# Kernel tuning notes

Measured on AMD Instinct MI355X. Metric: run time of the kernel, lower is better.

Reference implementation:

```python
import jax, jax.numpy as jnp
import numpy as np

N_PER_CLOUD = 2048   # points per cloud (batch entries are equal-sized, sorted)
NUM_CLOUDS = 8       # batch_size constant in the source module
RADIUS = 0.2         # init arg r
MAX_NEIGHBORS = 32   # init arg max_neighbors
F_IN, H1, H2, F_OUT = 3, 64, 64, 128  # PointNet++ SA MLP widths; nn input = F_IN + 3


def setup_inputs() -> dict:
    key = jax.random.key(0)
    ks = jax.random.split(key, 8)
    N = NUM_CLOUDS * N_PER_CLOUD
    x = jax.random.normal(ks[0], (N, F_IN), dtype=jnp.float32)
    pos = jax.random.uniform(ks[1], (N, 3), dtype=jnp.float32)  # unit cube
    batch = jnp.repeat(jnp.arange(NUM_CLOUDS, dtype=jnp.int32), N_PER_CLOUD)
    d_in = F_IN + 3
    W1 = jax.random.normal(ks[2], (d_in, H1), dtype=jnp.float32) / np.sqrt(d_in)
    b1 = jnp.zeros((H1,), dtype=jnp.float32)
    W2 = jax.random.normal(ks[3], (H1, H2), dtype=jnp.float32) / np.sqrt(H1)
    b2 = jnp.zeros((H2,), dtype=jnp.float32)
    W3 = jax.random.normal(ks[4], (H2, F_OUT), dtype=jnp.float32) / np.sqrt(H2)
    b3 = jnp.zeros((F_OUT,), dtype=jnp.float32)
    return dict(x=x, pos=pos, batch=batch, W1=W1, b1=b1, W2=W2, b2=b2, W3=W3, b3=b3)


def reference(x, pos, batch, W1, b1, W2, b2, W3, b3):
    N = pos.shape[0]
    B = N // N_PER_CLOUD
    n = N_PER_CLOUD
    posb = pos.reshape(B, n, 3)
    xb = x.reshape(B, n, -1)

    # --- radius ball query (per cloud, first MAX_NEIGHBORS in index order) ---
    diff = posb[:, :, None, :] - posb[:, None, :, :]          # [B, n_query, n_src, 3]
    d2 = jnp.sum(diff * diff, axis=-1)                        # [B, n, n]
    valid = d2 <= RADIUS * RADIUS                             # includes self -> >=1 nbr
    j_idx = jnp.arange(n, dtype=jnp.int32)
    keys = jnp.where(valid, j_idx[None, None, :], n)          # invalid -> sentinel n
    nbr = jnp.argsort(keys, axis=-1)[..., :MAX_NEIGHBORS]     # [B, n, K]
    nbr_ok = jnp.take_along_axis(keys, nbr, axis=-1) < n      # [B, n, K] bool

    # --- PointNetConv: msg = nn(cat([x_j, pos_j - pos_i])), max aggregation ---
    b_ix = jnp.arange(B)[:, None, None]
    x_j = xb[b_ix, nbr]                                        # [B, n, K, F_IN]
    rel = posb[b_ix, nbr] - posb[:, :, None, :]               # [B, n, K, 3]
    msg = jnp.concatenate([x_j, rel], axis=-1)                # [B, n, K, F_IN+3]
    h = jax.nn.relu(msg @ W1 + b1)
    h = jax.nn.relu(h @ W2 + b2)
    h = h @ W3 + b3                                           # [B, n, K, F_OUT]
    h = jnp.where(nbr_ok[..., None], h, -jnp.inf)
    out = jnp.max(h, axis=2).reshape(N, -1)                   # [N, F_OUT]
    return out, pos, batch
```

## Files before the change

### kernel.cpp

```cpp
#include <hip/hip_runtime.h>
#include <hip/hip_bf16.h>
#include <math.h>

#define NPC   2048
#define NC    8
#define NTOT  (NPC * NC)
#define KMAX  32
#define R2    0.04f

typedef short bf16x8  __attribute__((ext_vector_type(8)));
typedef float f32x16  __attribute__((ext_vector_type(16)));

__device__ __forceinline__ unsigned int f2bf(float f) {
    unsigned int u = __float_as_uint(f);
    return (u + 0x7FFFu + ((u >> 16) & 1u)) >> 16;
}

__device__ __forceinline__ unsigned int pkbf(float a, float b) {
    unsigned int r;
    asm("v_cvt_pk_bf16_f32 %0, %1, %2" : "=v"(r) : "v"(a), "v"(b));
    return r;
}

__device__ __forceinline__ int mbcnt64(unsigned long long m) {
    return (int)__builtin_amdgcn_mbcnt_hi((unsigned int)(m >> 32),
            __builtin_amdgcn_mbcnt_lo((unsigned int)m, 0u));
}

__device__ __forceinline__ bf16x8 mk_frag(const f32x16& a, int off) {
    int4 w;
    w.x = (int)pkbf(fmaxf(a[off+0],0.f), fmaxf(a[off+1],0.f));
    w.y = (int)pkbf(fmaxf(a[off+2],0.f), fmaxf(a[off+3],0.f));
    w.z = (int)pkbf(fmaxf(a[off+4],0.f), fmaxf(a[off+5],0.f));
    w.w = (int)pkbf(fmaxf(a[off+6],0.f), fmaxf(a[off+7],0.f));
    return __builtin_bit_cast(bf16x8, w);
}

__global__ __launch_bounds__(512) void prep_small(
    const float* __restrict__ pos, const int* __restrict__ batch,
    const float* __restrict__ W1, const float* __restrict__ b1,
    const float* __restrict__ W2, const float* __restrict__ b2,
    const float* __restrict__ W3,
    unsigned short* __restrict__ wf, float* __restrict__ out)
{
    int b = blockIdx.x, tid = threadIdx.x;
    if (b < 28) {
        int g = b * 512 + tid;
        if (g < 1024) {
            int j = g & 7, lane = (g >> 3) & 63, t = g >> 9;
            int k = (lane >> 5)*8 + j, ch = t*32 + (lane & 31);
            float v = (k < 6) ? W1[k*64 + ch] : (k == 6 ? b1[ch] : 0.f);
            wf[g] = (unsigned short)f2bf(v);
        } else if (g < 6144) {
            int g2 = g - 1024;
            int j = g2 & 7, lane = (g2 >> 3) & 63, f = g2 >> 9;
            int t = f / 5, kk = f % 5;
            int hi = lane >> 5, row = t*32 + (lane & 31);
            float v;
            if (kk < 4) {
                int k = (j & 3) + 4*hi + 8*(2*(kk & 1) + (j >> 2)) + 32*(kk >> 1);
                v = W2[k*64 + row];
            } else {
                v = (hi == 0 && j == 0) ? b2[row] : 0.f;
            }
            wf[g] = (unsigned short)f2bf(v);
        } else {
            int g3 = g - 6144;
            int j = g3 & 7, lane = (g3 >> 3) & 63, f = g3 >> 9;
            int n = f >> 2, kk = f & 3;
            int hi = lane >> 5, col = n*32 + (lane & 31);
            int k = (j & 3) + 4*hi + 8*(2*(kk & 1) + (j >> 2)) + 32*(kk >> 1);
            wf[g] = (unsigned short)f2bf(W3[k*128 + col]);
        }
    } else {
        int i = (b - 28) * 512 + tid;
        if (i < NTOT*3) out[NTOT*128 + i] = pos[i];
        else            out[NTOT*131 + (i - NTOT*3)] = (float)batch[i - NTOT*3];
    }
}

__global__ __launch_bounds__(1024, 8) void fused_kernel(
    const float* __restrict__ x, const float* __restrict__ pos,
    const unsigned short* __restrict__ wf, const float* __restrict__ b3,
    float* __restrict__ out)
{
    __shared__ float2 sPxy[NPC];
    __shared__ float  sPz[NPC];
    __shared__ int4   sW[1664];
    __shared__ int    snbr[16*32];

    const int tid  = threadIdx.x;
    const int lane = tid & 63, wave = tid >> 6;
    const int e = lane & 31, hi = lane >> 5;
    const int q     = blockIdx.x * 16 + wave;
    const int base  = (q >> 11) << 11;
    const int ql    = q - base;

    if (tid < 512) {
        const float4* src = (const float4*)(pos + 3*base);
        float4 f0 = src[3*tid], f1 = src[3*tid+1], f2 = src[3*tid+2];
        sPxy[4*tid+0] = make_float2(f0.x, f0.y); sPz[4*tid+0] = f0.z;
        sPxy[4*tid+1] = make_float2(f0.w, f1.x); sPz[4*tid+1] = f1.y;
        sPxy[4*tid+2] = make_float2(f1.z, f1.w); sPz[4*tid+2] = f2.x;
        sPxy[4*tid+3] = make_float2(f2.y, f2.z); sPz[4*tid+3] = f2.w;
    } else {
        const int4* wsrc = (const int4*)(wf + 1024);
        int t = tid - 512;
        #pragma unroll
        for (int it = 0; it < 4; ++it) {
            int idx = it*512 + t;
            if (idx < 1664) sW[idx] = wsrc[idx];
        }
    }
    bf16x8 wA1_0 = *(const bf16x8*)(wf + (0*64 + lane)*8);
    bf16x8 wA1_1 = *(const bf16x8*)(wf + (1*64 + lane)*8);
    float b3v[4];
    #pragma unroll
    for (int n = 0; n < 4; ++n) b3v[n] = b3[n*32 + e];
    __syncthreads();

    const float2 qxy = sPxy[ql];
    const float qx = qxy.x, qy = qxy.y, qz = sPz[ql];
    int cnt = 0;
    for (int j0 = 0; j0 < NPC && cnt < KMAX; j0 += 256) {
        unsigned long long ms[4];
        bool vs[4];
        #pragma unroll
        for (int s = 0; s < 4; ++s) {
            int j = j0 + s*64 + lane;
            float2 pxy = sPxy[j];
            float  pz  = sPz[j];
            float dx = __fsub_rn(pxy.x, qx);
            float dy = __fsub_rn(pxy.y, qy);
            float dz = __fsub_rn(pz,    qz);
            float d2 = __fadd_rn(__fadd_rn(__fmul_rn(dx,dx), __fmul_rn(dy,dy)),
                                 __fmul_rn(dz,dz));
            vs[s] = d2 <= R2;
            ms[s] = __ballot(vs[s]);
        }
        #pragma unroll
        for (int s = 0; s < 4; ++s) {
            int slot = cnt + mbcnt64(ms[s]);
            if (vs[s] && slot < KMAX) snbr[(wave << 5) + slot] = j0 + s*64 + lane;
            cnt += (int)__popcll(ms[s]);
        }
    }
    if (cnt > KMAX) cnt = KMAX;

    int jl = (e < cnt) ? snbr[(wave << 5) + e] : ql;
    float2 pjxy = sPxy[jl];
    float  pjz  = sPz[jl];
    float xj0 = x[3*(base + jl)], xj1 = x[3*(base + jl) + 1], xj2 = x[3*(base + jl) + 2];

    const unsigned int one_w = pkbf(1.0f, 0.0f);
    int4 ow = {0,0,0,0};
    if (!hi) ow.x = (int)one_w;
    const bf16x8 onef = __builtin_bit_cast(bf16x8, ow);

    float r0 = pjxy.x - qx, r1 = pjxy.y - qy, r2 = pjz - qz;
    int4 mw;
    mw.x = hi ? 0 : (int)pkbf(xj0, xj1);
    mw.y = hi ? 0 : (int)pkbf(xj2, r0);
    mw.z = hi ? 0 : (int)pkbf(r1, r2);
    mw.w = hi ? 0 : (int)one_w;
    bf16x8 msgf = __builtin_bit_cast(bf16x8, mw);

    __builtin_amdgcn_s_setprio(1);
    f32x16 acc0 = {}, acc1 = {};
    acc0 = __builtin_amdgcn_mfma_f32_32x32x16_bf16(wA1_0, msgf, acc0, 0, 0, 0);
    acc1 = __builtin_amdgcn_mfma_f32_32x32x16_bf16(wA1_1, msgf, acc1, 0, 0, 0);
    __builtin_amdgcn_s_setprio(0);
    bf16x8 h1f[4];
    h1f[0] = mk_frag(acc0, 0);
    h1f[1] = mk_frag(acc0, 8);
    h1f[2] = mk_frag(acc1, 0);
    h1f[3] = mk_frag(acc1, 8);

    __builtin_amdgcn_s_setprio(1);
    f32x16 c20 = {}, c21 = {};
    #pragma unroll
    for (int kk = 0; kk < 4; ++kk) {
        c20 = __builtin_amdgcn_mfma_f32_32x32x16_bf16(
                *(const bf16x8*)&sW[(0*5 + kk)*64 + lane], h1f[kk], c20, 0, 0, 0);
        c21 = __builtin_amdgcn_mfma_f32_32x32x16_bf16(
                *(const bf16x8*)&sW[(1*5 + kk)*64 + lane], h1f[kk], c21, 0, 0, 0);
    }
    c20 = __builtin_amdgcn_mfma_f32_32x32x16_bf16(
            *(const bf16x8*)&sW[(0*5 + 4)*64 + lane], onef, c20, 0, 0, 0);
    c21 = __builtin_amdgcn_mfma_f32_32x32x16_bf16(
            *(const bf16x8*)&sW[(1*5 + 4)*64 + lane], onef, c21, 0, 0, 0);
    __builtin_amdgcn_s_setprio(0);
    bf16x8 h2f[4];
    h2f[0] = mk_frag(c20, 0);
    h2f[1] = mk_frag(c20, 8);
    h2f[2] = mk_frag(c21, 0);
    h2f[3] = mk_frag(c21, 8);

    const bool full = (cnt == 32);
    #pragma unroll
    for (int n = 0; n < 4; ++n) {
        __builtin_amdgcn_s_setprio(1);
        f32x16 c = {};
        #pragma unroll
        for (int kk = 0; kk < 4; ++kk)
            c = __builtin_amdgcn_mfma_f32_32x32x16_bf16(
                    h2f[kk], *(const bf16x8*)&sW[640 + (n*4 + kk)*64 + lane], c, 0, 0, 0);
        __builtin_amdgcn_s_setprio(0);
        float m;
        if (full) {
            float t0 = fmaxf(fmaxf(c[0],  c[1]),  c[2]);
            float t1 = fmaxf(fmaxf(c[3],  c[4]),  c[5]);
            float t2 = fmaxf(fmaxf(c[6],  c[7]),  c[8]);
            float t3 = fmaxf(fmaxf(c[9],  c[10]), c[11]);
            float t4 = fmaxf(fmaxf(c[12], c[13]), c[14]);
            m = fmaxf(fmaxf(t0, t1), c[15]);
            m = fmaxf(fmaxf(m, t2), t3);
            m = fmaxf(m, t4);
        } else {
            m = -INFINITY;
            #pragma unroll
            for (int reg = 0; reg < 16; ++reg) {
                int r = (reg & 3) + 8*(reg >> 2) + 4*hi;
                m = fmaxf(m, (r < cnt) ? c[reg] : -INFINITY);
            }
        }
        m = fmaxf(m, __shfl_xor(m, 32));
        m += b3v[n];
        if (hi == 0) out[q*128 + n*32 + e] = m;
    }
}

extern "C" void kernel_launch(void* const* d_in, const int* in_sizes, int n_in,
                              void* d_out, int out_size, void* d_ws, size_t ws_size,
                              hipStream_t stream) {
    const float* x     = (const float*)d_in[0];
    const float* pos   = (const float*)d_in[1];
    const int*   batch = (const int*)d_in[2];
    const float* W1    = (const float*)d_in[3];
    const float* b1    = (const float*)d_in[4];
    const float* W2    = (const float*)d_in[5];
    const float* b2    = (const float*)d_in[6];
    const float* W3    = (const float*)d_in[7];
    const float* b3    = (const float*)d_in[8];
    float* out = (float*)d_out;

    unsigned short* wfrag = (unsigned short*)d_ws;

    prep_small<<<156, 512, 0, stream>>>(pos, batch, W1, b1, W2, b2, W3, wfrag, out);
    fused_kernel<<<1024, 1024, 0, stream>>>(x, pos, wfrag, b3, out);
}
```

Baseline: 34.92 us.

## Process two queries per wave and halve block count with paired point layout

Result: slower. 92.56 us (+165.1%).

```diff
diff --git a/kernel.cpp b/kernel.cpp
--- a/kernel.cpp
+++ b/kernel.cpp
@@ -84,25 +84,25 @@
     const unsigned short* __restrict__ wf, const float* __restrict__ b3,
     float* __restrict__ out)
 {
-    __shared__ float2 sPxy[NPC];
-    __shared__ float  sPz[NPC];
+    __shared__ float4 sPxy4[NPC/2];
+    __shared__ float2 sPz2[NPC/2];
     __shared__ int4   sW[1664];
-    __shared__ int    snbr[16*32];
+    __shared__ int    snbr[16*64];
 
     const int tid  = threadIdx.x;
     const int lane = tid & 63, wave = tid >> 6;
     const int e = lane & 31, hi = lane >> 5;
-    const int q     = blockIdx.x * 16 + wave;
-    const int base  = (q >> 11) << 11;
-    const int ql    = q - base;
+    const int q0    = __builtin_amdgcn_readfirstlane(blockIdx.x * 32 + wave * 2);
+    const int base  = (q0 >> 11) << 11;
+    const int q0l   = q0 - base;
 
     if (tid < 512) {
         const float4* src = (const float4*)(pos + 3*base);
         float4 f0 = src[3*tid], f1 = src[3*tid+1], f2 = src[3*tid+2];
-        sPxy[4*tid+0] = make_float2(f0.x, f0.y); sPz[4*tid+0] = f0.z;
-        sPxy[4*tid+1] = make_float2(f0.w, f1.x); sPz[4*tid+1] = f1.y;
-        sPxy[4*tid+2] = make_float2(f1.z, f1.w); sPz[4*tid+2] = f2.x;
-        sPxy[4*tid+3] = make_float2(f2.y, f2.z); sPz[4*tid+3] = f2.w;
+        sPxy4[2*tid+0] = make_float4(f0.x, f0.y, f0.w, f1.x);
+        sPz2 [2*tid+0] = make_float2(f0.z, f1.y);
+        sPxy4[2*tid+1] = make_float4(f1.z, f1.w, f2.y, f2.z);
+        sPz2 [2*tid+1] = make_float2(f2.x, f2.w);
     } else {
         const int4* wsrc = (const int4*)(wf + 1024);
         int t = tid - 512;
@@ -119,115 +119,137 @@
     for (int n = 0; n < 4; ++n) b3v[n] = b3[n*32 + e];
     __syncthreads();
 
-    const float2 qxy = sPxy[ql];
-    const float qx = qxy.x, qy = qxy.y, qz = sPz[ql];
-    int cnt = 0;
-    for (int j0 = 0; j0 < NPC && cnt < KMAX; j0 += 256) {
-        unsigned long long ms[4];
-        bool vs[4];
-        #pragma unroll
-        for (int s = 0; s < 4; ++s) {
-            int j = j0 + s*64 + lane;
-            float2 pxy = sPxy[j];
-            float  pz  = sPz[j];
-            float dx = __fsub_rn(pxy.x, qx);
-            float dy = __fsub_rn(pxy.y, qy);
-            float dz = __fsub_rn(pz,    qz);
-            float d2 = __fadd_rn(__fadd_rn(__fmul_rn(dx,dx), __fmul_rn(dy,dy)),
-                                 __fmul_rn(dz,dz));
-            vs[s] = d2 <= R2;
-            ms[s] = __ballot(vs[s]);
-        }
-        #pragma unroll
-        for (int s = 0; s < 4; ++s) {
-            int slot = cnt + mbcnt64(ms[s]);
-            if (vs[s] && slot < KMAX) snbr[(wave << 5) + slot] = j0 + s*64 + lane;
-            cnt += (int)__popcll(ms[s]);
+    const float4 qv = sPxy4[q0l >> 1];
+    const float2 qzv = sPz2[q0l >> 1];
+    const float q0x = qv.x, q0y = qv.y, q0z = qzv.x;
+    const float q1x = qv.z, q1y = qv.w, q1z = qzv.y;
+
+    int cnt0 = 0, cnt1 = 0;
+    for (int j0 = 0; j0 < NPC && (cnt0 < KMAX || cnt1 < KMAX); j0 += 128) {
+        float4 pp = sPxy4[(j0 >> 1) + lane];
+        float2 zz = sPz2[(j0 >> 1) + lane];
+        if (cnt0 < KMAX) {
+            float dax = __fsub_rn(pp.x, q0x), day = __fsub_rn(pp.y, q0y), daz = __fsub_rn(zz.x, q0z);
+            float dbx = __fsub_rn(pp.z, q0x), dby = __fsub_rn(pp.w, q0y), dbz = __fsub_rn(zz.y, q0z);
+            float d2a = __fadd_rn(__fadd_rn(__fmul_rn(dax,dax), __fmul_rn(day,day)), __fmul_rn(daz,daz));
+            float d2b = __fadd_rn(__fadd_rn(__fmul_rn(dbx,dbx), __fmul_rn(dby,dby)), __fmul_rn(dbz,dbz));
+            bool va = d2a <= R2, vb = d2b <= R2;
+            unsigned long long me = __ballot(va), mo = __ballot(vb);
+            int se = cnt0 + mbcnt64(me) + mbcnt64(mo);
+            int so = se + (va ? 1 : 0);
+            if (va && se < KMAX) snbr[(wave << 6) + se] = j0 + 2*lane;
+            if (vb && so < KMAX) snbr[(wave << 6) + so] = j0 + 2*lane + 1;
+            cnt0 += (int)__popcll(me) + (int)__popcll(mo);
+        }
+        if (cnt1 < KMAX) {
+            float dax = __fsub_rn(pp.x, q1x), day = __fsub_rn(pp.y, q1y), daz = __fsub_rn(zz.x, q1z);
+            float dbx = __fsub_rn(pp.z, q1x), dby = __fsub_rn(pp.w, q1y), dbz = __fsub_rn(zz.y, q1z);
+            float d2a = __fadd_rn(__fadd_rn(__fmul_rn(dax,dax), __fmul_rn(day,day)), __fmul_rn(daz,daz));
+            float d2b = __fadd_rn(__fadd_rn(__fmul_rn(dbx,dbx), __fmul_rn(dby,dby)), __fmul_rn(dbz,dbz));
+            bool va = d2a <= R2, vb = d2b <= R2;
+            unsigned long long me = __ballot(va), mo = __ballot(vb);
+            int se = cnt1 + mbcnt64(me) + mbcnt64(mo);
+            int so = se + (va ? 1 : 0);
+            if (va && se < KMAX) snbr[(wave << 6) + 32 + se] = j0 + 2*lane;
+            if (vb && so < KMAX) snbr[(wave << 6) + 32 + so] = j0 + 2*lane + 1;
+            cnt1 += (int)__popcll(me) + (int)__popcll(mo);
         }
     }
-    if (cnt > KMAX) cnt = KMAX;
-
-    int jl = (e < cnt) ? snbr[(wave << 5) + e] : ql;
-    float2 pjxy = sPxy[jl];
-    float  pjz  = sPz[jl];
-    float xj0 = x[3*(base + jl)], xj1 = x[3*(base + jl) + 1], xj2 = x[3*(base + jl) + 2];
+    if (cnt0 > KMAX) cnt0 = KMAX;
+    if (cnt1 > KMAX) cnt1 = KMAX;
 
     const unsigned int one_w = pkbf(1.0f, 0.0f);
     int4 ow = {0,0,0,0};
     if (!hi) ow.x = (int)one_w;
     const bf16x8 onef = __builtin_bit_cast(bf16x8, ow);
 
-    float r0 = pjxy.x - qx, r1 = pjxy.y - qy, r2 = pjz - qz;
-    int4 mw;
-    mw.x = hi ? 0 : (int)pkbf(xj0, xj1);
-    mw.y = hi ? 0 : (int)pkbf(xj2, r0);
-    mw.z = hi ? 0 : (int)pkbf(r1, r2);
-    mw.w = hi ? 0 : (int)one_w;
-    bf16x8 msgf = __builtin_bit_cast(bf16x8, mw);
-
-    __builtin_amdgcn_s_setprio(1);
-    f32x16 acc0 = {}, acc1 = {};
-    acc0 = __builtin_amdgcn_mfma_f32_32x32x16_bf16(wA1_0, msgf, acc0, 0, 0, 0);
-    acc1 = __builtin_amdgcn_mfma_f32_32x32x16_bf16(wA1_1, msgf, acc1, 0, 0, 0);
-    __builtin_amdgcn_s_setprio(0);
-    bf16x8 h1f[4];
-    h1f[0] = mk_frag(acc0, 0);
-    h1f[1] = mk_frag(acc0, 8);
-    h1f[2] = mk_frag(acc1, 0);
-    h1f[3] = mk_frag(acc1, 8);
-
-    __builtin_amdgcn_s_setprio(1);
-    f32x16 c20 = {}, c21 = {};
-    #pragma unroll
-    for (int kk = 0; kk < 4; ++kk) {
+    auto MLP = [&](int q, int ql, int cnt, int nbase, float qx, float qy, float qz) {
+        int jl = (e < cnt) ? snbr[nbase + e] : ql;
+        float4 pv = sPxy4[jl >> 1];
+        float2 zv = sPz2[jl >> 1];
+        bool odd = (jl & 1) != 0;
+        float pjx = odd ? pv.z : pv.x;
+        float pjy = odd ? pv.w : pv.y;
+        float pjz = odd ? zv.y : zv.x;
+        int gj = base + jl;
+        float xj0 = x[3*gj], xj1 = x[3*gj+1], xj2 = x[3*gj+2];
+
+        float r0 = pjx - qx, r1 = pjy - qy, r2 = pjz - qz;
+        int4 mw;
+        mw.x = hi ? 0 : (int)pkbf(xj0, xj1);
+        mw.y = hi ? 0 : (int)pkbf(xj2, r0);
+        mw.z = hi ? 0 : (int)pkbf(r1, r2);
+        mw.w = hi ? 0 : (int)one_w;
+        bf16x8 msgf = __builtin_bit_cast(bf16x8, mw);
+
+        __builtin_amdgcn_s_setprio(1);
+        f32x16 acc0 = {}, acc1 = {};
+        acc0 = __builtin_amdgcn_mfma_f32_32x32x16_bf16(wA1_0, msgf, acc0, 0, 0, 0);
+        acc1 = __builtin_amdgcn_mfma_f32_32x32x16_bf16(wA1_1, msgf, acc1, 0, 0, 0);
+        __builtin_amdgcn_s_setprio(0);
+        bf16x8 h1f[4];
+        h1f[0] = mk_frag(acc0, 0);
+        h1f[1] = mk_frag(acc0, 8);
+        h1f[2] = mk_frag(acc1, 0);
+        h1f[3] = mk_frag(acc1, 8);
+
+        __builtin_amdgcn_s_setprio(1);
+        f32x16 c20 = {}, c21 = {};
+        #pragma unroll
+        for (int kk = 0; kk < 4; ++kk) {
+            c20 = __builtin_amdgcn_mfma_f32_32x32x16_bf16(
+                    *(const bf16x8*)&sW[(0*5 + kk)*64 + lane], h1f[kk], c20, 0, 0, 0);
+            c21 = __builtin_amdgcn_mfma_f32_32x32x16_bf16(
+                    *(const bf16x8*)&sW[(1*5 + kk)*64 + lane], h1f[kk], c21, 0, 0, 0);
+        }
         c20 = __builtin_amdgcn_mfma_f32_32x32x16_bf16(
-                *(const bf16x8*)&sW[(0*5 + kk)*64 + lane], h1f[kk], c20, 0, 0, 0);
+                *(const bf16x8*)&sW[(0*5 + 4)*64 + lane], onef, c20, 0, 0, 0);
         c21 = __builtin_amdgcn_mfma_f32_32x32x16_bf16(
-                *(const bf16x8*)&sW[(1*5 + kk)*64 + lane], h1f[kk], c21, 0, 0, 0);
-    }
-    c20 = __builtin_amdgcn_mfma_f32_32x32x16_bf16(
-            *(const bf16x8*)&sW[(0*5 + 4)*64 + lane], onef, c20, 0, 0, 0);
-    c21 = __builtin_amdgcn_mfma_f32_32x32x16_bf16(
-            *(const bf16x8*)&sW[(1*5 + 4)*64 + lane], onef, c21, 0, 0, 0);
-    __builtin_amdgcn_s_setprio(0);
-    bf16x8 h2f[4];
-    h2f[0] = mk_frag(c20, 0);
-    h2f[1] = mk_frag(c20, 8);
-    h2f[2] = mk_frag(c21, 0);
-    h2f[3] = mk_frag(c21, 8);
-
-    const bool full = (cnt == 32);
-    #pragma unroll
-    for (int n = 0; n < 4; ++n) {
-        __builtin_amdgcn_s_setprio(1);
-        f32x16 c = {};
+                *(const bf16x8*)&sW[(1*5 + 4)*64 + lane], onef, c21, 0, 0, 0);
+        __builtin_amdgcn_s_setprio(0);
+        bf16x8 h2f[4];
+        h2f[0] = mk_frag(c20, 0);
+        h2f[1] = mk_frag(c20, 8);
+        h2f[2] = mk_frag(c21, 0);
+        h2f[3] = mk_frag(c21, 8);
+
+        const bool full = (cnt == 32);
         #pragma unroll
-        for (int kk = 0; kk < 4; ++kk)
-            c = __builtin_amdgcn_mfma_f32_32x32x16_bf16(
-                    h2f[kk], *(const bf16x8*)&sW[640 + (n*4 + kk)*64 + lane], c, 0, 0, 0);
-        __builtin_amdgcn_s_setprio(0);
-        float m;
-        if (full) {
-            float t0 = fmaxf(fmaxf(c[0],  c[1]),  c[2]);
-            float t1 = fmaxf(fmaxf(c[3],  c[4]),  c[5]);
-            float t2 = fmaxf(fmaxf(c[6],  c[7]),  c[8]);
-            float t3 = fmaxf(fmaxf(c[9],  c[10]), c[11]);
-            float t4 = fmaxf(fmaxf(c[12], c[13]), c[14]);
-            m = fmaxf(fmaxf(t0, t1), c[15]);
-            m = fmaxf(fmaxf(m, t2), t3);
-            m = fmaxf(m, t4);
-        } else {
-            m = -INFINITY;
+        for (int n = 0; n < 4; ++n) {
+            f32x16 c;
             #pragma unroll
-            for (int reg = 0; reg < 16; ++reg) {
-                int r = (reg & 3) + 8*(reg >> 2) + 4*hi;
-                m = fmaxf(m, (r < cnt) ? c[reg] : -INFINITY);
+            for (int r = 0; r < 16; ++r) c[r] = b3v[n];
+            __builtin_amdgcn_s_setprio(1);
+            #pragma unroll
+            for (int kk = 0; kk < 4; ++kk)
+                c = __builtin_amdgcn_mfma_f32_32x32x16_bf16(
+                        h2f[kk], *(const bf16x8*)&sW[640 + (n*4 + kk)*64 + lane], c, 0, 0, 0);
+            __builtin_amdgcn_s_setprio(0);
+            float m;
+            if (full) {
+                float t0 = fmaxf(fmaxf(c[0],  c[1]),  c[2]);
+                float t1 = fmaxf(fmaxf(c[3],  c[4]),  c[5]);
+                float t2 = fmaxf(fmaxf(c[6],  c[7]),  c[8]);
+                float t3 = fmaxf(fmaxf(c[9],  c[10]), c[11]);
+                float t4 = fmaxf(fmaxf(c[12], c[13]), c[14]);
+                m = fmaxf(fmaxf(t0, t1), c[15]);
+                m = fmaxf(fmaxf(m, t2), t3);
+                m = fmaxf(m, t4);
+            } else {
+                m = -INFINITY;
+                #pragma unroll
+                for (int reg = 0; reg < 16; ++reg) {
+                    int r = (reg & 3) + 8*(reg >> 2) + 4*hi;
+                    m = fmaxf(m, (r < cnt) ? c[reg] : -INFINITY);
+                }
             }
-        }
-        m = fmaxf(m, __shfl_xor(m, 32));
-        m += b3v[n];
-        if (hi == 0) out[q*128 + n*32 + e] = m;
-    }
+            m = fmaxf(m, __shfl_xor(m, 32));
+            if (hi == 0) out[q*128 + n*32 + e] = m;
+        }
+    };
+
+    MLP(q0,     q0l,     cnt0, (wave << 6),      q0x, q0y, q0z);
+    MLP(q0 + 1, q0l + 1, cnt1, (wave << 6) + 32, q1x, q1y, q1z);
 }
 
 extern "C" void kernel_launch(void* const* d_in, const int* in_sizes, int n_in,
@@ -247,5 +269,5 @@
     unsigned short* wfrag = (unsigned short*)d_ws;
 
     prep_small<<<156, 512, 0, stream>>>(pos, batch, W1, b1, W2, b2, W3, wfrag, out);
-    fused_kernel<<<1024, 1024, 0, stream>>>(x, pos, wfrag, b3, out);
-}
+    fused_kernel<<<NTOT / 32, 1024, 0, stream>>>(x, pos, wfrag, b3, out);
+}
```

## Process two query points per wave to amortize per-block shared loads

Applied to the files above, without the earlier changes.

Measured after the change: 39.86 us. 1.14x slower.

```diff
diff --git a/kernel.cpp b/kernel.cpp
--- a/kernel.cpp
+++ b/kernel.cpp
@@ -79,6 +79,112 @@
     }
 }
 
+#define SEARCH_BODY(QX, QY, QZ, CNT, NOFF)                                              \
+    {                                                                                   \
+        for (int j0 = 0; j0 < NPC && CNT < KMAX; j0 += 256) {                           \
+            unsigned long long ms_[4];                                                  \
+            bool vs_[4];                                                                \
+            _Pragma("unroll")                                                           \
+            for (int s = 0; s < 4; ++s) {                                               \
+                int j = j0 + s*64 + lane;                                               \
+                float2 pxy = sPxy[j];                                                   \
+                float  pz  = sPz[j];                                                    \
+                float dx = __fsub_rn(pxy.x, QX);                                        \
+                float dy = __fsub_rn(pxy.y, QY);                                        \
+                float dz = __fsub_rn(pz,    QZ);                                        \
+                float d2 = __fadd_rn(__fadd_rn(__fmul_rn(dx,dx), __fmul_rn(dy,dy)),     \
+                                     __fmul_rn(dz,dz));                                 \
+                vs_[s] = d2 <= R2;                                                      \
+                ms_[s] = __ballot(vs_[s]);                                              \
+            }                                                                           \
+            _Pragma("unroll")                                                           \
+            for (int s = 0; s < 4; ++s) {                                               \
+                int slot = CNT + mbcnt64(ms_[s]);                                       \
+                if (vs_[s] && slot < KMAX) snbr[(NOFF) + slot] = j0 + s*64 + lane;      \
+                CNT += (int)__popcll(ms_[s]);                                           \
+            }                                                                           \
+        }                                                                               \
+        if (CNT > KMAX) CNT = KMAX;                                                     \
+    }
+
+#define MLP_BODY(Q, QL, CNT, NOFF, QX, QY, QZ)                                          \
+    {                                                                                   \
+        int jl = (e < CNT) ? snbr[(NOFF) + e] : (QL);                                   \
+        float2 pjxy = sPxy[jl];                                                         \
+        float  pjz  = sPz[jl];                                                          \
+        int gj = base + jl;                                                             \
+        float xj0 = x[3*gj], xj1 = x[3*gj+1], xj2 = x[3*gj+2];                          \
+        float r0 = pjxy.x - (QX), r1 = pjxy.y - (QY), r2 = pjz - (QZ);                  \
+        int4 mw;                                                                        \
+        mw.x = hi ? 0 : (int)pkbf(xj0, xj1);                                            \
+        mw.y = hi ? 0 : (int)pkbf(xj2, r0);                                             \
+        mw.z = hi ? 0 : (int)pkbf(r1, r2);                                              \
+        mw.w = hi ? 0 : (int)one_w;                                                     \
+        bf16x8 msgf = __builtin_bit_cast(bf16x8, mw);                                   \
+        __builtin_amdgcn_s_setprio(1);                                                  \
+        f32x16 acc0 = {}, acc1 = {};                                                    \
+        acc0 = __builtin_amdgcn_mfma_f32_32x32x16_bf16(wA1_0, msgf, acc0, 0, 0, 0);     \
+        acc1 = __builtin_amdgcn_mfma_f32_32x32x16_bf16(wA1_1, msgf, acc1, 0, 0, 0);     \
+        __builtin_amdgcn_s_setprio(0);                                                  \
+        bf16x8 h1f[4];                                                                  \
+        h1f[0] = mk_frag(acc0, 0);                                                      \
+        h1f[1] = mk_frag(acc0, 8);                                                      \
+        h1f[2] = mk_frag(acc1, 0);                                                      \
+        h1f[3] = mk_frag(acc1, 8);                                                      \
+        __builtin_amdgcn_s_setprio(1);                                                  \
+        f32x16 c20 = {}, c21 = {};                                                      \
+        _Pragma("unroll")                                                               \
+        for (int kk = 0; kk < 4; ++kk) {                                                \
+            c20 = __builtin_amdgcn_mfma_f32_32x32x16_bf16(                              \
+                    *(const bf16x8*)&sW[(0*5 + kk)*64 + lane], h1f[kk], c20, 0, 0, 0);  \
+            c21 = __builtin_amdgcn_mfma_f32_32x32x16_bf16(                              \
+                    *(const bf16x8*)&sW[(1*5 + kk)*64 + lane], h1f[kk], c21, 0, 0, 0);  \
+        }                                                                               \
+        c20 = __builtin_amdgcn_mfma_f32_32x32x16_bf16(                                  \
+                *(const bf16x8*)&sW[(0*5 + 4)*64 + lane], onef, c20, 0, 0, 0);          \
+        c21 = __builtin_amdgcn_mfma_f32_32x32x16_bf16(                                  \
+                *(const bf16x8*)&sW[(1*5 + 4)*64 + lane], onef, c21, 0, 0, 0);          \
+        __builtin_amdgcn_s_setprio(0);                                                  \
+        bf16x8 h2f[4];                                                                  \
+        h2f[0] = mk_frag(c20, 0);                                                       \
+        h2f[1] = mk_frag(c20, 8);                                                       \
+        h2f[2] = mk_frag(c21, 0);                                                       \
+        h2f[3] = mk_frag(c21, 8);                                                       \
+        const bool full = (CNT == 32);                                                  \
+        _Pragma("unroll")                                                               \
+        for (int n = 0; n < 4; ++n) {                                                   \
+            __builtin_amdgcn_s_setprio(1);                                              \
+            f32x16 c = {};                                                              \
+            _Pragma("unroll")                                                           \
+            for (int kk = 0; kk < 4; ++kk)                                              \
+                c = __builtin_amdgcn_mfma_f32_32x32x16_bf16(                            \
+                        h2f[kk], *(const bf16x8*)&sW[640 + (n*4 + kk)*64 + lane],       \
+                        c, 0, 0, 0);                                                    \
+            __builtin_amdgcn_s_setprio(0);                                              \
+            float m;                                                                    \
+            if (full) {                                                                 \
+                float t0 = fmaxf(fmaxf(c[0],  c[1]),  c[2]);                            \
+                float t1 = fmaxf(fmaxf(c[3],  c[4]),  c[5]);                            \
+                float t2 = fmaxf(fmaxf(c[6],  c[7]),  c[8]);                            \
+                float t3 = fmaxf(fmaxf(c[9],  c[10]), c[11]);                           \
+                float t4 = fmaxf(fmaxf(c[12], c[13]), c[14]);                           \
+                m = fmaxf(fmaxf(t0, t1), c[15]);                                        \
+                m = fmaxf(fmaxf(m, t2), t3);                                            \
+                m = fmaxf(m, t4);                                                       \
+            } else {                                                                    \
+                m = -INFINITY;                                                          \
+                _Pragma("unroll")                                                       \
+                for (int reg = 0; reg < 16; ++reg) {                                    \
+                    int r = (reg & 3) + 8*(reg >> 2) + 4*hi;                            \
+                    m = fmaxf(m, (r < CNT) ? c[reg] : -INFINITY);                       \
+                }                                                                       \
+            }                                                                           \
+            m = fmaxf(m, __shfl_xor(m, 32));                                            \
+            m += b3v[n];                                                                \
+            if (hi == 0) out[(Q)*128 + n*32 + e] = m;                                   \
+        }                                                                               \
+    }
+
 __global__ __launch_bounds__(1024, 8) void fused_kernel(
     const float* __restrict__ x, const float* __restrict__ pos,
     const unsigned short* __restrict__ wf, const float* __restrict__ b3,
@@ -87,14 +193,15 @@
     __shared__ float2 sPxy[NPC];
     __shared__ float  sPz[NPC];
     __shared__ int4   sW[1664];
-    __shared__ int    snbr[16*32];
+    __shared__ int    snbr[16*64];
 
     const int tid  = threadIdx.x;
     const int lane = tid & 63, wave = tid >> 6;
     const int e = lane & 31, hi = lane >> 5;
-    const int q     = blockIdx.x * 16 + wave;
-    const int base  = (q >> 11) << 11;
-    const int ql    = q - base;
+    const int q0    = __builtin_amdgcn_readfirstlane(blockIdx.x * 32 + wave * 2);
+    const int base  = (q0 >> 11) << 11;
+    const int q0l   = q0 - base;
+    const int woff  = wave << 6;
 
     if (tid < 512) {
         const float4* src = (const float4*)(pos + 3*base);
@@ -119,115 +226,23 @@
     for (int n = 0; n < 4; ++n) b3v[n] = b3[n*32 + e];
     __syncthreads();
 
-    const float2 qxy = sPxy[ql];
-    const float qx = qxy.x, qy = qxy.y, qz = sPz[ql];
-    int cnt = 0;
-    for (int j0 = 0; j0 < NPC && cnt < KMAX; j0 += 256) {
-        unsigned long long ms[4];
-        bool vs[4];
-        #pragma unroll
-        for (int s = 0; s < 4; ++s) {
-            int j = j0 + s*64 + lane;
-            float2 pxy = sPxy[j];
-            float  pz  = sPz[j];
-            float dx = __fsub_rn(pxy.x, qx);
-            float dy = __fsub_rn(pxy.y, qy);
-            float dz = __fsub_rn(pz,    qz);
-            float d2 = __fadd_rn(__fadd_rn(__fmul_rn(dx,dx), __fmul_rn(dy,dy)),
-                                 __fmul_rn(dz,dz));
-            vs[s] = d2 <= R2;
-            ms[s] = __ballot(vs[s]);
-        }
-        #pragma unroll
-        for (int s = 0; s < 4; ++s) {
-            int slot = cnt + mbcnt64(ms[s]);
-            if (vs[s] && slot < KMAX) snbr[(wave << 5) + slot] = j0 + s*64 + lane;
-            cnt += (int)__popcll(ms[s]);
-        }
-    }
-    if (cnt > KMAX) cnt = KMAX;
-
-    int jl = (e < cnt) ? snbr[(wave << 5) + e] : ql;
-    float2 pjxy = sPxy[jl];
-    float  pjz  = sPz[jl];
-    float xj0 = x[3*(base + jl)], xj1 = x[3*(base + jl) + 1], xj2 = x[3*(base + jl) + 2];
-
     const unsigned int one_w = pkbf(1.0f, 0.0f);
     int4 ow = {0,0,0,0};
     if (!hi) ow.x = (int)one_w;
     const bf16x8 onef = __builtin_bit_cast(bf16x8, ow);
 
-    float r0 = pjxy.x - qx, r1 = pjxy.y - qy, r2 = pjz - qz;
-    int4 mw;
-    mw.x = hi ? 0 : (int)pkbf(xj0, xj1);
-    mw.y = hi ? 0 : (int)pkbf(xj2, r0);
-    mw.z = hi ? 0 : (int)pkbf(r1, r2);
-    mw.w = hi ? 0 : (int)one_w;
-    bf16x8 msgf = __builtin_bit_cast(bf16x8, mw);
-
-    __builtin_amdgcn_s_setprio(1);
-    f32x16 acc0 = {}, acc1 = {};
-    acc0 = __builtin_amdgcn_mfma_f32_32x32x16_bf16(wA1_0, msgf, acc0, 0, 0, 0);
-    acc1 = __builtin_amdgcn_mfma_f32_32x32x16_bf16(wA1_1, msgf, acc1, 0, 0, 0);
-    __builtin_amdgcn_s_setprio(0);
-    bf16x8 h1f[4];
-    h1f[0] = mk_frag(acc0, 0);
-    h1f[1] = mk_frag(acc0, 8);
-    h1f[2] = mk_frag(acc1, 0);
-    h1f[3] = mk_frag(acc1, 8);
-
-    __builtin_amdgcn_s_setprio(1);
-    f32x16 c20 = {}, c21 = {};
-    #pragma unroll
-    for (int kk = 0; kk < 4; ++kk) {
-        c20 = __builtin_amdgcn_mfma_f32_32x32x16_bf16(
-                *(const bf16x8*)&sW[(0*5 + kk)*64 + lane], h1f[kk], c20, 0, 0, 0);
-        c21 = __builtin_amdgcn_mfma_f32_32x32x16_bf16(
-                *(const bf16x8*)&sW[(1*5 + kk)*64 + lane], h1f[kk], c21, 0, 0, 0);
-    }
-    c20 = __builtin_amdgcn_mfma_f32_32x32x16_bf16(
-            *(const bf16x8*)&sW[(0*5 + 4)*64 + lane], onef, c20, 0, 0, 0);
-    c21 = __builtin_amdgcn_mfma_f32_32x32x16_bf16(
-            *(const bf16x8*)&sW[(1*5 + 4)*64 + lane], onef, c21, 0, 0, 0);
-    __builtin_amdgcn_s_setprio(0);
-    bf16x8 h2f[4];
-    h2f[0] = mk_frag(c20, 0);
-    h2f[1] = mk_frag(c20, 8);
-    h2f[2] = mk_frag(c21, 0);
-    h2f[3] = mk_frag(c21, 8);
-
-    const bool full = (cnt == 32);
-    #pragma unroll
-    for (int n = 0; n < 4; ++n) {
-        __builtin_amdgcn_s_setprio(1);
-        f32x16 c = {};
-        #pragma unroll
-        for (int kk = 0; kk < 4; ++kk)
-            c = __builtin_amdgcn_mfma_f32_32x32x16_bf16(
-                    h2f[kk], *(const bf16x8*)&sW[640 + (n*4 + kk)*64 + lane], c, 0, 0, 0);
-        __builtin_amdgcn_s_setprio(0);
-        float m;
-        if (full) {
-            float t0 = fmaxf(fmaxf(c[0],  c[1]),  c[2]);
-            float t1 = fmaxf(fmaxf(c[3],  c[4]),  c[5]);
-            float t2 = fmaxf(fmaxf(c[6],  c[7]),  c[8]);
-            float t3 = fmaxf(fmaxf(c[9],  c[10]), c[11]);
-            float t4 = fmaxf(fmaxf(c[12], c[13]), c[14]);
-            m = fmaxf(fmaxf(t0, t1), c[15]);
-            m = fmaxf(fmaxf(m, t2), t3);
-            m = fmaxf(m, t4);
-        } else {
-            m = -INFINITY;
-            #pragma unroll
-            for (int reg = 0; reg < 16; ++reg) {
-                int r = (reg & 3) + 8*(reg >> 2) + 4*hi;
-                m = fmaxf(m, (r < cnt) ? c[reg] : -INFINITY);
-            }
-        }
-        m = fmaxf(m, __shfl_xor(m, 32));
-        m += b3v[n];
-        if (hi == 0) out[q*128 + n*32 + e] = m;
-    }
+    const float2 q0xy = sPxy[q0l];
+    const float q0x = q0xy.x, q0y = q0xy.y, q0z = sPz[q0l];
+    const float2 q1xy = sPxy[q0l + 1];
+    const float q1x = q1xy.x, q1y = q1xy.y, q1z = sPz[q0l + 1];
+
+    int cnt0 = 0;
+    SEARCH_BODY(q0x, q0y, q0z, cnt0, woff)
+    MLP_BODY(q0, q0l, cnt0, woff, q0x, q0y, q0z)
+
+    int cnt1 = 0;
+    SEARCH_BODY(q1x, q1y, q1z, cnt1, woff + 32)
+    MLP_BODY(q0 + 1, q0l + 1, cnt1, woff + 32, q1x, q1y, q1z)
 }
 
 extern "C" void kernel_launch(void* const* d_in, const int* in_sizes, int n_in,
@@ -247,5 +262,5 @@
     unsigned short* wfrag = (unsigned short*)d_ws;
 
     prep_small<<<156, 512, 0, stream>>>(pos, batch, W1, b1, W2, b2, W3, wfrag, out);
-    fused_kernel<<<1024, 1024, 0, stream>>>(x, pos, wfrag, b3, out);
-}
+    fused_kernel<<<NTOT / 32, 1024, 0, stream>>>(x, pos, wfrag, b3, out);
+}
```
